# Optimization experiments

Measured on AMD Instinct MI355X. Metric: run time of the kernel, lower is better.

## Reference

```python
import jax, jax.numpy as jnp
import numpy as np

BS, SLEN, EM = 32, 4096, 256


def setup_inputs() -> dict:
    key = jax.random.key(0)
    ks = jax.random.split(key, 8)
    word_embedded = jax.random.normal(ks[0], (BS, SLEN, EM), dtype=jnp.float32)
    # valid-token mask: first `length` tokens valid per row (True = keep)
    lengths = jax.random.randint(ks[1], (BS, 1), SLEN // 2, SLEN + 1)
    mask = jnp.arange(SLEN)[None, :] < lengths  # (BS, SLEN) bool
    s = 1.0 / np.sqrt(EM)
    w_query = jax.random.uniform(ks[2], (EM, 1), minval=-1.0, maxval=1.0, dtype=jnp.float32)  # Linear(1, em, bias=False)
    wq = jax.random.uniform(ks[3], (EM, EM), minval=-s, maxval=s, dtype=jnp.float32)
    bq = jax.random.uniform(ks[4], (EM,), minval=-s, maxval=s, dtype=jnp.float32)
    wk = jax.random.uniform(ks[5], (EM, EM), minval=-s, maxval=s, dtype=jnp.float32)
    bk = jax.random.uniform(ks[6], (EM,), minval=-s, maxval=s, dtype=jnp.float32)
    se = 1.0 / np.sqrt(2 * EM)
    we = jax.random.uniform(ks[7], (1, 2 * EM), minval=-se, maxval=se, dtype=jnp.float32)
    be = jnp.zeros((1,), dtype=jnp.float32)
    return {"word_embedded": word_embedded, "mask": mask, "w_query": w_query,
            "wq": wq, "bq": bq, "wk": wk, "bk": bk, "we": we, "be": be}


def reference(word_embedded, mask, w_query, wq, bq, wk, bk, we, be):
    bs, slen, em = word_embedded.shape
    # query = Linear(1, em, no bias) applied to ones -> each row is w_query[:, 0]
    q = jnp.broadcast_to(w_query[:, 0], (bs, em))          # (bs, em)
    qp = jax.nn.relu(q @ wq.T + bq)                        # (bs, em); dropout is identity at eval
    k = jax.nn.relu(word_embedded @ wk.T + bk)             # (bs, slen, em)
    # proj_e(tanh(cat(q, k))) == tanh(q)@we_q + tanh(k)@we_k + be (tanh is elementwise),
    # so we avoid materializing the (bs, slen, 2*em) concat.
    we_q, we_k = we[0, :em], we[0, em:]
    energy = jnp.tanh(qp) @ we_q                           # (bs,)
    energy = energy[:, None] + jnp.tanh(k) @ we_k + be[0]  # (bs, slen)
    # torch: energy.masked_fill_(~mask, 1e-45)
    energy = jnp.where(mask, energy, jnp.float32(1e-45))
    attn_weights = jax.nn.softmax(energy, axis=1)          # (bs, slen)
    sent_embedded = jnp.einsum('bs,bse->be', attn_weights, word_embedded)  # (bs, em)
    return sent_embedded
```

## Files before the change

### kernel.cpp

```cpp
#include <hip/hip_runtime.h>

#define BS   32
#define SLEN 4096
#define EM   256
#define NROWS (BS * SLEN)

typedef __attribute__((ext_vector_type(8))) short bf16x8;
typedef __attribute__((ext_vector_type(4))) float f32x4;

#define WS_WKB   0
#define WS_EN    32768
#define WS_CONST 163840
#define WS_W     163856
#define WS_PART  294928

__device__ inline short f2bf(float x) {
  union { float f; unsigned u; } v; v.f = x;
  unsigned r = v.u + 0x7fffu + ((v.u >> 16) & 1u);
  return (short)(r >> 16);
}

__device__ inline float tanh_pos(float x) {
  float e2 = __expf(2.f * x);
  return 1.f - __fdividef(2.f, e2 + 1.f);
}

__global__ __launch_bounds__(256) void k0_cvt(const float* __restrict__ wk,
                                              unsigned short* __restrict__ wkb) {
  int idx = (blockIdx.x * 256 + threadIdx.x) * 4;
  float4 v = *(const float4*)(wk + idx);
  ushort4 o;
  o.x = (unsigned short)f2bf(v.x);
  o.y = (unsigned short)f2bf(v.y);
  o.z = (unsigned short)f2bf(v.z);
  o.w = (unsigned short)f2bf(v.w);
  *(ushort4*)(wkb + idx) = o;
}

__global__ __launch_bounds__(256) void k0b_qscalar(const float* __restrict__ w_query,
                                                   const float* __restrict__ wq,
                                                   const float* __restrict__ bq,
                                                   const float* __restrict__ we,
                                                   const float* __restrict__ be,
                                                   float* __restrict__ outc) {
  int t = threadIdx.x;
  float a = 0.f;
  const float* row = wq + (size_t)t * EM;
#pragma unroll 8
  for (int j = 0; j < EM; ++j) a = fmaf(row[j], w_query[j], a);
  a += bq[t];
  float v = we[t] * tanh_pos(fmaxf(a, 0.f));
#pragma unroll
  for (int off = 32; off >= 1; off >>= 1) v += __shfl_xor(v, off, 64);
  __shared__ float red[4];
  if ((t & 63) == 0) red[t >> 6] = v;
  __syncthreads();
  if (t == 0) outc[0] = red[0] + red[1] + red[2] + red[3] + be[0];
}

__global__ __launch_bounds__(256) void k1_energy(const float* __restrict__ X,
                                                 const unsigned short* __restrict__ wkb,
                                                 const float* __restrict__ bk,
                                                 const float* __restrict__ we,
                                                 float* __restrict__ energy) {
  __shared__ float ep[64][2];
  const int tid = threadIdx.x;
  const int l = tid & 63;
  const int wid = tid >> 6;
  const int wr = wid >> 1, wc = wid & 1;
  const int lr = l & 15, lk = l >> 4;
  const int row0 = blockIdx.x * 64;
  const float* xw = X + (size_t)(row0 + wr * 32 + lr) * EM;
  const unsigned short* bw = wkb + (size_t)(wc * 128 + lr) * EM;

  f32x4 acc[2][8];
#pragma unroll
  for (int i = 0; i < 2; ++i)
#pragma unroll
    for (int n = 0; n < 8; ++n) acc[i][n] = (f32x4){0.f, 0.f, 0.f, 0.f};

#pragma unroll
  for (int s = 0; s < 8; ++s) {
    const int kf = s * 32 + lk * 8;
    bf16x8 af[2];
#pragma unroll
    for (int i = 0; i < 2; ++i) {
      const float* src = xw + (size_t)(i * 16) * EM + kf;
      float4 v0 = *(const float4*)src;
      float4 v1 = *(const float4*)(src + 4);
      bf16x8 t;
      t[0] = f2bf(v0.x); t[1] = f2bf(v0.y); t[2] = f2bf(v0.z); t[3] = f2bf(v0.w);
      t[4] = f2bf(v1.x); t[5] = f2bf(v1.y); t[6] = f2bf(v1.z); t[7] = f2bf(v1.w);
      af[i] = t;
    }
    bf16x8 bfr[8];
#pragma unroll
    for (int n = 0; n < 8; ++n)
      bfr[n] = *(const bf16x8*)(bw + (size_t)(n * 16) * EM + kf);
#pragma unroll
    for (int i = 0; i < 2; ++i)
#pragma unroll
      for (int n = 0; n < 8; ++n)
        acc[i][n] = __builtin_amdgcn_mfma_f32_16x16x32_bf16(af[i], bfr[n], acc[i][n], 0, 0, 0);
  }

  float bkv[8], wev[8];
#pragma unroll
  for (int n = 0; n < 8; ++n) {
    int e = wc * 128 + n * 16 + lr;
    bkv[n] = bk[e];
    wev[n] = we[EM + e];
  }
#pragma unroll
  for (int i = 0; i < 2; ++i) {
#pragma unroll
    for (int r = 0; r < 4; ++r) {
      float p = 0.f;
#pragma unroll
      for (int n = 0; n < 8; ++n) {
        float kv = fmaxf(acc[i][n][r] + bkv[n], 0.f);
        p += wev[n] * tanh_pos(kv);
      }
#pragma unroll
      for (int off = 1; off <= 8; off <<= 1) p += __shfl_xor(p, off, 64);
      if (lr == 0) ep[wr * 32 + i * 16 + lk * 4 + r][wc] = p;
    }
  }
  __syncthreads();
  if (tid < 64) energy[row0 + tid] = ep[tid][0] + ep[tid][1];
}

__global__ __launch_bounds__(256) void k2_softmax(const float* __restrict__ energy,
                                                  const unsigned char* __restrict__ mask,
                                                  const float* __restrict__ cptr,
                                                  float* __restrict__ wout) {
  const int b = blockIdx.x;
  const int t = threadIdx.x;
  const float C = cptr[0];
  const bool mask_is_byte = (mask[1] | mask[2] | mask[3]) != 0;
  const int* mask32 = (const int*)mask;
  const float* eb = energy + (size_t)b * SLEN;
  float v[16];
  float m = -3.4e38f;
#pragma unroll
  for (int i = 0; i < 16; ++i) {
    int s = t + i * 256;
    int mv = mask_is_byte ? (int)mask[(size_t)b * SLEN + s]
                          : mask32[(size_t)b * SLEN + s];
    float x = mv ? (eb[s] + C) : 1.4012984643248171e-45f;
    v[i] = x;
    m = fmaxf(m, x);
  }
  __shared__ float red[8];
#pragma unroll
  for (int off = 32; off >= 1; off >>= 1) m = fmaxf(m, __shfl_xor(m, off, 64));
  if ((t & 63) == 0) red[t >> 6] = m;
  __syncthreads();
  m = fmaxf(fmaxf(red[0], red[1]), fmaxf(red[2], red[3]));
  float s_ = 0.f;
#pragma unroll
  for (int i = 0; i < 16; ++i) {
    v[i] = __expf(v[i] - m);
    s_ += v[i];
  }
#pragma unroll
  for (int off = 32; off >= 1; off >>= 1) s_ += __shfl_xor(s_, off, 64);
  if ((t & 63) == 0) red[4 + (t >> 6)] = s_;
  __syncthreads();
  float inv = 1.f / (red[4] + red[5] + red[6] + red[7]);
  float* wb = wout + (size_t)b * SLEN;
#pragma unroll
  for (int i = 0; i < 16; ++i) wb[t + i * 256] = v[i] * inv;
}

__global__ __launch_bounds__(256) void k3_wsum(const float* __restrict__ X,
                                               const float* __restrict__ w,
                                               float* __restrict__ part) {
  __shared__ float red[4][EM];
  const int b = blockIdx.x >> 5;
  const int ch = blockIdx.x & 31;
  const int g = threadIdx.x >> 6;
  const int l = threadIdx.x & 63;
  const int s0 = ch * 128 + g * 32;
  const float* xb = X + (size_t)b * SLEN * EM;
  const float* wb = w + (size_t)b * SLEN;
  float4 acc = make_float4(0.f, 0.f, 0.f, 0.f);
#pragma unroll 4
  for (int i = 0; i < 32; ++i) {
    int s = s0 + i;
    float ws_ = wb[s];
    float4 v = *(const float4*)(xb + (size_t)s * EM + l * 4);
    acc.x = fmaf(ws_, v.x, acc.x);
    acc.y = fmaf(ws_, v.y, acc.y);
    acc.z = fmaf(ws_, v.z, acc.z);
    acc.w = fmaf(ws_, v.w, acc.w);
  }
  *(float4*)(&red[g][l * 4]) = acc;
  __syncthreads();
  if (g == 0) {
    float4 r0 = *(const float4*)(&red[0][l * 4]);
    float4 r1 = *(const float4*)(&red[1][l * 4]);
    float4 r2 = *(const float4*)(&red[2][l * 4]);
    float4 r3 = *(const float4*)(&red[3][l * 4]);
    float4 o;
    o.x = (r0.x + r1.x) + (r2.x + r3.x);
    o.y = (r0.y + r1.y) + (r2.y + r3.y);
    o.z = (r0.z + r1.z) + (r2.z + r3.z);
    o.w = (r0.w + r1.w) + (r2.w + r3.w);
    *(float4*)(part + (size_t)(b * 32 + ch) * EM + l * 4) = o;
  }
}

__global__ __launch_bounds__(256) void k4_reduce(const float* __restrict__ part,
                                                 float* __restrict__ out) {
  const int b = blockIdx.x;
  const int e = threadIdx.x;
  float s = 0.f;
#pragma unroll 8
  for (int k = 0; k < 32; ++k) s += part[((size_t)b * 32 + k) * EM + e];
  out[(size_t)b * EM + e] = s;
}

extern "C" void kernel_launch(void* const* d_in, const int* in_sizes, int n_in,
                              void* d_out, int out_size, void* d_ws, size_t ws_size,
                              hipStream_t stream) {
  const float* X = (const float*)d_in[0];
  const unsigned char* mask = (const unsigned char*)d_in[1];
  const float* w_query = (const float*)d_in[2];
  const float* wq = (const float*)d_in[3];
  const float* bq = (const float*)d_in[4];
  const float* wk = (const float*)d_in[5];
  const float* bk = (const float*)d_in[6];
  const float* we = (const float*)d_in[7];
  const float* be = (const float*)d_in[8];
  float* out = (float*)d_out;
  float* ws = (float*)d_ws;

  unsigned short* wkb = (unsigned short*)(ws + WS_WKB);
  float* energy = ws + WS_EN;
  float* cscalar = ws + WS_CONST;
  float* weights = ws + WS_W;
  float* part = ws + WS_PART;

  k0_cvt<<<64, 256, 0, stream>>>(wk, wkb);
  k0b_qscalar<<<1, 256, 0, stream>>>(w_query, wq, bq, we, be, cscalar);
  k1_energy<<<NROWS / 64, 256, 0, stream>>>(X, wkb, bk, we, energy);
  k2_softmax<<<BS, 256, 0, stream>>>(energy, mask, cscalar, weights);
  k3_wsum<<<BS * 32, 256, 0, stream>>>(X, weights, part);
  k4_reduce<<<BS, 256, 0, stream>>>(part, out);
}
```

Baseline: 321.4 us.

## Stage energy GEMM through double-buffered LDS with async weight loads

The energy GEMM now repacks Wk into a k-chunk-major bf16 layout, streams it into LDS with global_load_lds, and stages converted X tiles in a swizzled, double-buffered LDS buffer. The next chunk is prefetched while the current MFMAs run. The bias is folded into the accumulator init and the tanh epilogue is rewritten as sum(w) - 2w/(e^{2x}+1). The weighted-sum kernel is split into twice as many blocks, with a matching partial reduction. This aims to cut redundant per-wave global loads of Wk and hide load latency, at the cost of more LDS use and block-wide syncs.

```diff
diff --git a/kernel.cpp b/kernel.cpp
--- a/kernel.cpp
+++ b/kernel.cpp
@@ -20,21 +20,22 @@
   return (short)(r >> 16);
 }
 
-__device__ inline float tanh_pos(float x) {
-  float e2 = __expf(2.f * x);
-  return 1.f - __fdividef(2.f, e2 + 1.f);
-}
+#define GLOAD_LDS16(g, l)                                                  \
+  __builtin_amdgcn_global_load_lds(                                        \
+      (const __attribute__((address_space(1))) unsigned int*)(g),          \
+      (__attribute__((address_space(3))) unsigned int*)(l), 16, 0, 0)
 
 __global__ __launch_bounds__(256) void k0_cvt(const float* __restrict__ wk,
-                                              unsigned short* __restrict__ wkb) {
-  int idx = (blockIdx.x * 256 + threadIdx.x) * 4;
-  float4 v = *(const float4*)(wk + idx);
-  ushort4 o;
-  o.x = (unsigned short)f2bf(v.x);
-  o.y = (unsigned short)f2bf(v.y);
-  o.z = (unsigned short)f2bf(v.z);
-  o.w = (unsigned short)f2bf(v.w);
-  *(ushort4*)(wkb + idx) = o;
+                                              unsigned short* __restrict__ wkb2) {
+  int gid = blockIdx.x * 256 + threadIdx.x;
+  int e = gid >> 5, kq = gid & 31;
+  const float* src = wk + (size_t)e * EM + kq * 8;
+  float4 v0 = *(const float4*)src;
+  float4 v1 = *(const float4*)(src + 4);
+  bf16x8 pk;
+  pk[0] = f2bf(v0.x); pk[1] = f2bf(v0.y); pk[2] = f2bf(v0.z); pk[3] = f2bf(v0.w);
+  pk[4] = f2bf(v1.x); pk[5] = f2bf(v1.y); pk[6] = f2bf(v1.z); pk[7] = f2bf(v1.w);
+  *(bf16x8*)(wkb2 + ((size_t)kq * 256 + e) * 8) = pk;
 }
 
 __global__ __launch_bounds__(256) void k0b_qscalar(const float* __restrict__ w_query,
@@ -44,12 +45,21 @@
                                                    const float* __restrict__ be,
                                                    float* __restrict__ outc) {
   int t = threadIdx.x;
-  float a = 0.f;
   const float* row = wq + (size_t)t * EM;
+  float4 a4 = make_float4(0.f, 0.f, 0.f, 0.f);
 #pragma unroll 8
-  for (int j = 0; j < EM; ++j) a = fmaf(row[j], w_query[j], a);
-  a += bq[t];
-  float v = we[t] * tanh_pos(fmaxf(a, 0.f));
+  for (int j = 0; j < 64; ++j) {
+    float4 r = *(const float4*)(row + j * 4);
+    float4 q = *(const float4*)(w_query + j * 4);
+    a4.x = fmaf(r.x, q.x, a4.x);
+    a4.y = fmaf(r.y, q.y, a4.y);
+    a4.z = fmaf(r.z, q.z, a4.z);
+    a4.w = fmaf(r.w, q.w, a4.w);
+  }
+  float a = (a4.x + a4.y) + (a4.z + a4.w) + bq[t];
+  float kv = fmaxf(a, 0.f);
+  float z = __expf(kv + kv);
+  float v = we[t] * (1.f - __fdividef(2.f, z + 1.f));
 #pragma unroll
   for (int off = 32; off >= 1; off >>= 1) v += __shfl_xor(v, off, 64);
   __shared__ float red[4];
@@ -59,50 +69,21 @@
 }
 
 __global__ __launch_bounds__(256) void k1_energy(const float* __restrict__ X,
-                                                 const unsigned short* __restrict__ wkb,
+                                                 const unsigned short* __restrict__ wkb2,
                                                  const float* __restrict__ bk,
                                                  const float* __restrict__ we,
                                                  float* __restrict__ energy) {
-  __shared__ float ep[64][2];
+  __shared__ char lds[41472];
+  char* As = lds;
+  char* Bs = lds + 8192;
+  float* ep = (float*)(lds + 40960);
   const int tid = threadIdx.x;
   const int l = tid & 63;
   const int wid = tid >> 6;
   const int wr = wid >> 1, wc = wid & 1;
   const int lr = l & 15, lk = l >> 4;
   const int row0 = blockIdx.x * 64;
-  const float* xw = X + (size_t)(row0 + wr * 32 + lr) * EM;
-  const unsigned short* bw = wkb + (size_t)(wc * 128 + lr) * EM;
-
-  f32x4 acc[2][8];
-#pragma unroll
-  for (int i = 0; i < 2; ++i)
-#pragma unroll
-    for (int n = 0; n < 8; ++n) acc[i][n] = (f32x4){0.f, 0.f, 0.f, 0.f};
-
-#pragma unroll
-  for (int s = 0; s < 8; ++s) {
-    const int kf = s * 32 + lk * 8;
-    bf16x8 af[2];
-#pragma unroll
-    for (int i = 0; i < 2; ++i) {
-      const float* src = xw + (size_t)(i * 16) * EM + kf;
-      float4 v0 = *(const float4*)src;
-      float4 v1 = *(const float4*)(src + 4);
-      bf16x8 t;
-      t[0] = f2bf(v0.x); t[1] = f2bf(v0.y); t[2] = f2bf(v0.z); t[3] = f2bf(v0.w);
-      t[4] = f2bf(v1.x); t[5] = f2bf(v1.y); t[6] = f2bf(v1.z); t[7] = f2bf(v1.w);
-      af[i] = t;
-    }
-    bf16x8 bfr[8];
-#pragma unroll
-    for (int n = 0; n < 8; ++n)
-      bfr[n] = *(const bf16x8*)(bw + (size_t)(n * 16) * EM + kf);
-#pragma unroll
-    for (int i = 0; i < 2; ++i)
-#pragma unroll
-      for (int n = 0; n < 8; ++n)
-        acc[i][n] = __builtin_amdgcn_mfma_f32_16x16x32_bf16(af[i], bfr[n], acc[i][n], 0, 0, 0);
-  }
+  const int ar = tid >> 2, ac = tid & 3;
 
   float bkv[8], wev[8];
 #pragma unroll
@@ -111,23 +92,88 @@
     bkv[n] = bk[e];
     wev[n] = we[EM + e];
   }
+  f32x4 acc[2][8];
+#pragma unroll
+  for (int i = 0; i < 2; ++i)
+#pragma unroll
+    for (int n = 0; n < 8; ++n)
+      acc[i][n] = (f32x4){bkv[n], bkv[n], bkv[n], bkv[n]};
+
+#pragma unroll
+  for (int q = 0; q < 4; ++q) {
+    const char* g = (const char*)wkb2 + wid * 4096 + q * 1024 + l * 16;
+    GLOAD_LDS16(g, Bs + wid * 4096 + q * 1024);
+  }
+  {
+    const float* src = X + (size_t)(row0 + ar) * EM + ac * 8;
+    float4 a0 = *(const float4*)src;
+    float4 a1 = *(const float4*)(src + 4);
+    bf16x8 pk;
+    pk[0] = f2bf(a0.x); pk[1] = f2bf(a0.y); pk[2] = f2bf(a0.z); pk[3] = f2bf(a0.w);
+    pk[4] = f2bf(a1.x); pk[5] = f2bf(a1.y); pk[6] = f2bf(a1.z); pk[7] = f2bf(a1.w);
+    *(bf16x8*)(As + ar * 64 + ((ac ^ (ar & 3)) * 16)) = pk;
+  }
+  __syncthreads();
+
+#pragma unroll
+  for (int t = 0; t < 8; ++t) {
+    const int cur = t & 1, nxt = cur ^ 1;
+    float4 a0, a1;
+    if (t < 7) {
+#pragma unroll
+      for (int q = 0; q < 4; ++q) {
+        const char* g = (const char*)wkb2 + (t + 1) * 16384 + wid * 4096 + q * 1024 + l * 16;
+        GLOAD_LDS16(g, Bs + nxt * 16384 + wid * 4096 + q * 1024);
+      }
+      const float* src = X + (size_t)(row0 + ar) * EM + (t + 1) * 32 + ac * 8;
+      a0 = *(const float4*)src;
+      a1 = *(const float4*)(src + 4);
+    }
+    bf16x8 af[2], bfr[8];
+#pragma unroll
+    for (int i = 0; i < 2; ++i) {
+      int row = wr * 32 + i * 16 + lr;
+      af[i] = *(const bf16x8*)(As + cur * 4096 + row * 64 + ((lk ^ (row & 3)) * 16));
+    }
+#pragma unroll
+    for (int n = 0; n < 8; ++n)
+      bfr[n] = *(const bf16x8*)(Bs + cur * 16384 + lk * 4096 + (wc * 128 + n * 16 + lr) * 16);
+#pragma unroll
+    for (int i = 0; i < 2; ++i)
+#pragma unroll
+      for (int n = 0; n < 8; ++n)
+        acc[i][n] = __builtin_amdgcn_mfma_f32_16x16x32_bf16(af[i], bfr[n], acc[i][n], 0, 0, 0);
+    if (t < 7) {
+      bf16x8 pk;
+      pk[0] = f2bf(a0.x); pk[1] = f2bf(a0.y); pk[2] = f2bf(a0.z); pk[3] = f2bf(a0.w);
+      pk[4] = f2bf(a1.x); pk[5] = f2bf(a1.y); pk[6] = f2bf(a1.z); pk[7] = f2bf(a1.w);
+      *(bf16x8*)(As + nxt * 4096 + ar * 64 + ((ac ^ (ar & 3)) * 16)) = pk;
+    }
+    __syncthreads();
+  }
+
+  float sumw = 0.f, w2[8];
+#pragma unroll
+  for (int n = 0; n < 8; ++n) { sumw += wev[n]; w2[n] = -2.f * wev[n]; }
 #pragma unroll
   for (int i = 0; i < 2; ++i) {
 #pragma unroll
     for (int r = 0; r < 4; ++r) {
-      float p = 0.f;
+      float p = sumw;
 #pragma unroll
       for (int n = 0; n < 8; ++n) {
-        float kv = fmaxf(acc[i][n][r] + bkv[n], 0.f);
-        p += wev[n] * tanh_pos(kv);
+        float kv = fmaxf(acc[i][n][r], 0.f);
+        float z = __expf(kv + kv);
+        float rn = __fdividef(1.f, z + 1.f);
+        p = fmaf(w2[n], rn, p);
       }
 #pragma unroll
       for (int off = 1; off <= 8; off <<= 1) p += __shfl_xor(p, off, 64);
-      if (lr == 0) ep[wr * 32 + i * 16 + lk * 4 + r][wc] = p;
-    }
-  }
-  __syncthreads();
-  if (tid < 64) energy[row0 + tid] = ep[tid][0] + ep[tid][1];
+      if (lr == 0) ep[(wr * 32 + i * 16 + lk * 4 + r) * 2 + wc] = p;
+    }
+  }
+  __syncthreads();
+  if (tid < 64) energy[row0 + tid] = ep[tid * 2] + ep[tid * 2 + 1];
 }
 
 __global__ __launch_bounds__(256) void k2_softmax(const float* __restrict__ energy,
@@ -177,16 +223,16 @@
                                                const float* __restrict__ w,
                                                float* __restrict__ part) {
   __shared__ float red[4][EM];
-  const int b = blockIdx.x >> 5;
-  const int ch = blockIdx.x & 31;
+  const int b = blockIdx.x >> 6;
+  const int ch = blockIdx.x & 63;
   const int g = threadIdx.x >> 6;
   const int l = threadIdx.x & 63;
-  const int s0 = ch * 128 + g * 32;
+  const int s0 = ch * 64 + g * 16;
   const float* xb = X + (size_t)b * SLEN * EM;
   const float* wb = w + (size_t)b * SLEN;
   float4 acc = make_float4(0.f, 0.f, 0.f, 0.f);
-#pragma unroll 4
-  for (int i = 0; i < 32; ++i) {
+#pragma unroll
+  for (int i = 0; i < 16; ++i) {
     int s = s0 + i;
     float ws_ = wb[s];
     float4 v = *(const float4*)(xb + (size_t)s * EM + l * 4);
@@ -207,7 +253,7 @@
     o.y = (r0.y + r1.y) + (r2.y + r3.y);
     o.z = (r0.z + r1.z) + (r2.z + r3.z);
     o.w = (r0.w + r1.w) + (r2.w + r3.w);
-    *(float4*)(part + (size_t)(b * 32 + ch) * EM + l * 4) = o;
+    *(float4*)(part + (size_t)blockIdx.x * EM + l * 4) = o;
   }
 }
 
@@ -217,7 +263,7 @@
   const int e = threadIdx.x;
   float s = 0.f;
 #pragma unroll 8
-  for (int k = 0; k < 32; ++k) s += part[((size_t)b * 32 + k) * EM + e];
+  for (int k = 0; k < 64; ++k) s += part[((size_t)b * 64 + k) * EM + e];
   out[(size_t)b * EM + e] = s;
 }
 
@@ -236,16 +282,16 @@
   float* out = (float*)d_out;
   float* ws = (float*)d_ws;
 
-  unsigned short* wkb = (unsigned short*)(ws + WS_WKB);
+  unsigned short* wkb2 = (unsigned short*)(ws + WS_WKB);
   float* energy = ws + WS_EN;
   float* cscalar = ws + WS_CONST;
   float* weights = ws + WS_W;
   float* part = ws + WS_PART;
 
-  k0_cvt<<<64, 256, 0, stream>>>(wk, wkb);
+  k0_cvt<<<32, 256, 0, stream>>>(wk, wkb2);
   k0b_qscalar<<<1, 256, 0, stream>>>(w_query, wq, bq, we, be, cscalar);
-  k1_energy<<<NROWS / 64, 256, 0, stream>>>(X, wkb, bk, we, energy);
+  k1_energy<<<NROWS / 64, 256, 0, stream>>>(X, wkb2, bk, we, energy);
   k2_softmax<<<BS, 256, 0, stream>>>(energy, mask, cscalar, weights);
-  k3_wsum<<<BS * 32, 256, 0, stream>>>(X, weights, part);
+  k3_wsum<<<BS * 64, 256, 0, stream>>>(X, weights, part);
   k4_reduce<<<BS, 256, 0, stream>>>(part, out);
 }
```

Result: faster. 271.8 us (-15.4%).
